# Kernel optimization log

Hardware: AMD Instinct MI355X
Metric: run time of the kernel (lower is better)

Reference implementation:

```python
import jax, jax.numpy as jnp
import numpy as np

N = 256
WINDOW = 16
HORIZON = 12
STEPS_PER_WEEK = 4
DT = 1.0 / STEPS_PER_WEEK


def setup_inputs() -> dict:
    key = jax.random.key(0)
    ks = jax.random.split(key, 8)
    B = 512
    x_hist = jax.random.uniform(ks[0], (B, WINDOW, N), dtype=jnp.float32)
    cnn_feat = jax.random.normal(ks[1], (B, 64), dtype=jnp.float32)
    s = 0.02  # small init scale to keep sigmoids/softmax well-behaved
    W1 = jax.random.normal(ks[2], (WINDOW * N, 128), dtype=jnp.float32) * s
    b1 = jnp.zeros((128,), jnp.float32)
    W2 = jax.random.normal(ks[3], (128, 4 * N), dtype=jnp.float32) * s
    b2 = jnp.zeros((4 * N,), jnp.float32)
    M1 = jax.random.normal(ks[4], (64, 128), dtype=jnp.float32) * s
    mb1 = jnp.zeros((128,), jnp.float32)
    M2 = jax.random.normal(ks[5], (128, N * N), dtype=jnp.float32) * s
    mb2 = jnp.zeros((N * N,), jnp.float32)
    return {"x_hist": x_hist, "cnn_feat": cnn_feat, "W1": W1, "b1": b1,
            "W2": W2, "b2": b2, "M1": M1, "mb1": mb1, "M2": M2, "mb2": mb2}


def reference(x_hist, cnn_feat, W1, b1, W2, b2, M1, mb1, M2, mb2):
    B, T, n = x_hist.shape
    # param_net: Linear -> ReLU -> Linear
    h = jax.nn.relu(x_hist.reshape(B, -1) @ W1 + b1)
    params = h @ W2 + b2  # (B, 4N)
    beta = jax.nn.sigmoid(params[:, :n]) * 3.0
    sigma = jax.nn.sigmoid(params[:, n:2 * n]) * 1.0
    gamma = jax.nn.sigmoid(params[:, 2 * n:3 * n]) * 1.0
    e0_ratio = jax.nn.sigmoid(params[:, 3 * n:]) * 5.0
    # mobility_net -> row-softmax mobility matrix Pi (B, N, N)
    hm = jax.nn.relu(cnn_feat @ M1 + mb1)
    Pi = jax.nn.softmax((hm @ M2 + mb2).reshape(B, n, n), axis=-1)

    I0 = jnp.maximum(x_hist[:, -1], 1e-6)
    E0 = I0 * e0_ratio
    S0 = jnp.maximum(1.0 - E0 - I0, 0.01)

    def get_grads(S, E, I):
        # bmm(I[:,None,:], Pi).squeeze(1) == einsum bn,bnm->bm
        force = jnp.einsum('bn,bnm->bm', I, Pi)
        new_inf = beta * S * force
        return -new_inf, new_inf - sigma * E, sigma * E - gamma * I

    def week_step(carry, _):
        S, E, I = carry
        for _ in range(STEPS_PER_WEEK):
            dS1, dE1, dI1 = get_grads(S, E, I)
            dS2, dE2, dI2 = get_grads(S + 0.5 * DT * dS1, E + 0.5 * DT * dE1, I + 0.5 * DT * dI1)
            dS3, dE3, dI3 = get_grads(S + 0.5 * DT * dS2, E + 0.5 * DT * dE2, I + 0.5 * DT * dI2)
            dS4, dE4, dI4 = get_grads(S + DT * dS3, E + DT * dE3, I + DT * dI3)
            S = jnp.clip(S + DT / 6.0 * (dS1 + 2 * dS2 + 2 * dS3 + dS4), 0.0, 1.0)
            E = jnp.clip(E + DT / 6.0 * (dE1 + 2 * dE2 + 2 * dE3 + dE4), 0.0, 1.0)
            I = jnp.clip(I + DT / 6.0 * (dI1 + 2 * dI2 + 2 * dI3 + dI4), 0.0, 1.0)
        return (S, E, I), (I, E)

    _, (I_s, E_s) = jax.lax.scan(week_step, (S0, E0, I0), None, length=HORIZON)
    I_sim = jnp.swapaxes(I_s, 0, 1)  # (B, horizon, N)
    E_sim = jnp.swapaxes(E_s, 0, 1)
    return (I_sim, E_sim, beta.mean(0), sigma.mean(0), gamma.mean(0), Pi.mean(0))
```

## Files before the change

### kernel.cpp

```cpp
#include <hip/hip_runtime.h>
#include <hip/hip_bf16.h>
#include <stdint.h>
#include <stddef.h>

typedef _Float16 half2_t __attribute__((ext_vector_type(2)));
typedef _Float16 f16x8 __attribute__((ext_vector_type(8)));
typedef float f32x4 __attribute__((ext_vector_type(4)));

__device__ __forceinline__ float fdot2(half2_t a, half2_t b, float c) {
#if __has_builtin(__builtin_amdgcn_fdot2)
  return __builtin_amdgcn_fdot2(a, b, c, false);
#else
  return c + (float)a.x * (float)b.x + (float)a.y * (float)b.y;
#endif
}

__global__ __launch_bounds__(128) void k_paramnet1(
    const float* __restrict__ X, const float* __restrict__ W1,
    float* __restrict__ hpart) {
  const int j = threadIdx.x;
  const int ks = blockIdx.x;
  const int b0 = blockIdx.y * 32;

  float w1r[128];
#pragma unroll
  for (int k = 0; k < 128; ++k)
    w1r[k] = W1[(size_t)(ks * 128 + k) * 128 + j];

  for (int bb = 0; bb < 32; ++bb) {
    const float* xr = X + (size_t)(b0 + bb) * 4096 + ks * 128;
    float a0 = 0.f, a1 = 0.f, a2 = 0.f, a3 = 0.f;
#pragma unroll
    for (int k = 0; k < 128; k += 4) {
      a0 = fmaf(w1r[k + 0], xr[k + 0], a0);
      a1 = fmaf(w1r[k + 1], xr[k + 1], a1);
      a2 = fmaf(w1r[k + 2], xr[k + 2], a2);
      a3 = fmaf(w1r[k + 3], xr[k + 3], a3);
    }
    hpart[((size_t)ks * 512 + (b0 + bb)) * 128 + j] = (a0 + a1) + (a2 + a3);
  }
}

__global__ __launch_bounds__(256) void k_paramnet2(
    const float* __restrict__ hpart, const float* __restrict__ b1,
    float* __restrict__ h) {
  const int idx = blockIdx.x * 256 + threadIdx.x;
  float s = b1[idx & 127];
#pragma unroll
  for (int ks = 0; ks < 32; ++ks) s += hpart[(size_t)ks * 65536 + idx];
  h[idx] = fmaxf(s, 0.f);
}

__global__ __launch_bounds__(256) void k_params_state(
    const float* __restrict__ h, const float* __restrict__ W2,
    const float* __restrict__ b2, const float* __restrict__ X,
    float* __restrict__ betaW, float* __restrict__ sigmaW,
    float* __restrict__ gammaW, float* __restrict__ S0W,
    float* __restrict__ E0W, float* __restrict__ I0W,
    float* __restrict__ stats) {
  const int b0 = blockIdx.x * 2;
  const int t = threadIdx.x;
  const float* h0 = h + (size_t)b0 * 128;
  const float* h1 = h0 + 128;
  float a00 = b2[t], a01 = b2[256 + t], a02 = b2[512 + t], a03 = b2[768 + t];
  float a10 = a00, a11 = a01, a12 = a02, a13 = a03;
#pragma unroll 2
  for (int k = 0; k < 128; ++k) {
    const float* wr = W2 + (size_t)k * 1024;
    const float w0 = wr[t], w1 = wr[256 + t], w2 = wr[512 + t], w3 = wr[768 + t];
    const float hv0 = h0[k], hv1 = h1[k];
    a00 = fmaf(hv0, w0, a00); a01 = fmaf(hv0, w1, a01);
    a02 = fmaf(hv0, w2, a02); a03 = fmaf(hv0, w3, a03);
    a10 = fmaf(hv1, w0, a10); a11 = fmaf(hv1, w1, a11);
    a12 = fmaf(hv1, w2, a12); a13 = fmaf(hv1, w3, a13);
  }
  float bsum = 0.f, ssum = 0.f, gsum = 0.f;
#pragma unroll
  for (int j = 0; j < 2; ++j) {
    const float p0 = j ? a10 : a00, p1 = j ? a11 : a01;
    const float p2 = j ? a12 : a02, p3 = j ? a13 : a03;
    const float beta = 3.f / (1.f + __expf(-p0));
    const float sig  = 1.f / (1.f + __expf(-p1));
    const float gam  = 1.f / (1.f + __expf(-p2));
    const float e0r  = 5.f / (1.f + __expf(-p3));
    const int base = (b0 + j) * 256 + t;
    const float I0 = fmaxf(X[(size_t)(b0 + j) * 4096 + 15 * 256 + t], 1e-6f);
    const float E0 = I0 * e0r;
    const float S0 = fmaxf(1.f - E0 - I0, 0.01f);
    betaW[base] = beta; sigmaW[base] = sig; gammaW[base] = gam;
    S0W[base] = S0; E0W[base] = E0; I0W[base] = I0;
    bsum += beta; ssum += sig; gsum += gam;
  }
  atomicAdd(stats + t, bsum);
  atomicAdd(stats + 256 + t, ssum);
  atomicAdd(stats + 512 + t, gsum);
}

__global__ __launch_bounds__(128) void k_mobility1(
    const float* __restrict__ cnn, const float* __restrict__ M1,
    const float* __restrict__ mb1, _Float16* __restrict__ hmf) {
  const int b = blockIdx.x, j = threadIdx.x;
  const float* cr = cnn + b * 64;
  float a = mb1[j];
#pragma unroll
  for (int k = 0; k < 64; ++k) a = fmaf(cr[k], M1[k * 128 + j], a);
  hmf[b * 128 + j] = (_Float16)fmaxf(a, 0.f);
}

__global__ __launch_bounds__(256) void k_cvtM2(
    const float* __restrict__ M2, _Float16* __restrict__ M2T) {
  const int n = blockIdx.x, t = threadIdx.x;
  __shared__ _Float16 sm[128 * 256];
  const float* src = M2 + (size_t)n * 256 + t;
#pragma unroll 8
  for (int k = 0; k < 128; ++k)
    sm[k * 256 + t] = (_Float16)src[(size_t)k * 65536];
  __syncthreads();
  half2_t col[64];
#pragma unroll 16
  for (int k2 = 0; k2 < 64; ++k2)
    col[k2] = half2_t{sm[(2 * k2) * 256 + t], sm[(2 * k2 + 1) * 256 + t]};
  uint4* dst = (uint4*)(M2T + ((size_t)n * 256 + t) * 128);
  const uint4* s4 = (const uint4*)col;
#pragma unroll
  for (int i = 0; i < 16; ++i) dst[i] = s4[i];
}

__global__ __launch_bounds__(512, 2) void k_mobility2(
    const _Float16* __restrict__ hmf, const _Float16* __restrict__ M2T,
    const float* __restrict__ mb2, _Float16* __restrict__ PiF,
    float* __restrict__ pimpart) {
  const int n = blockIdx.x;
  const int pass = blockIdx.y;
  const int tid = threadIdx.x;
  const int wave = tid >> 6;
  const int lane = tid & 63;
  const int q = lane >> 4;
  const int c = lane & 15;

  __shared__ _Float16 sm[8][16 * 256];

  const _Float16* Bbase = M2T + (size_t)n * 32768 + (size_t)c * 128 + q * 8;
  const float* mbp = mb2 + n * 256 + c;

  const int bt0 = wave * 4 + pass * 2;
  f32x4 C0[16], C1[16];
#pragma unroll
  for (int nb = 0; nb < 16; ++nb) {
    const float mbv = mbp[nb * 16];
    C0[nb] = f32x4{mbv, mbv, mbv, mbv};
    C1[nb] = C0[nb];
  }
  const _Float16* A0 = hmf + (size_t)(bt0 * 16 + c) * 128 + q * 8;
  const _Float16* A1 = A0 + 16 * 128;
#pragma unroll
  for (int ks = 0; ks < 4; ++ks) {
    const f16x8 Af0 = *(const f16x8*)(A0 + ks * 32);
    const f16x8 Af1 = *(const f16x8*)(A1 + ks * 32);
#pragma unroll
    for (int nb = 0; nb < 16; ++nb) {
      const f16x8 Bf = *(const f16x8*)(Bbase + nb * 2048 + ks * 32);
      C0[nb] = __builtin_amdgcn_mfma_f32_16x16x32_f16(Af0, Bf, C0[nb], 0, 0, 0);
      C1[nb] = __builtin_amdgcn_mfma_f32_16x16x32_f16(Af1, Bf, C1[nb], 0, 0, 0);
    }
  }

  float colsum[16];
#pragma unroll
  for (int nb = 0; nb < 16; ++nb) colsum[nb] = 0.f;

#pragma unroll
  for (int half = 0; half < 2; ++half) {
    f32x4* C = half ? C1 : C0;
    const int bt = bt0 + half;
    float mx[4], sum[4];
#pragma unroll
    for (int r = 0; r < 4; ++r) mx[r] = C[0][r];
#pragma unroll
    for (int nb = 1; nb < 16; ++nb)
#pragma unroll
      for (int r = 0; r < 4; ++r) mx[r] = fmaxf(mx[r], C[nb][r]);
#pragma unroll
    for (int r = 0; r < 4; ++r) {
      mx[r] = fmaxf(mx[r], __shfl_xor(mx[r], 1, 16));
      mx[r] = fmaxf(mx[r], __shfl_xor(mx[r], 2, 16));
      mx[r] = fmaxf(mx[r], __shfl_xor(mx[r], 4, 16));
      mx[r] = fmaxf(mx[r], __shfl_xor(mx[r], 8, 16));
      sum[r] = 0.f;
    }
#pragma unroll
    for (int nb = 0; nb < 16; ++nb)
#pragma unroll
      for (int r = 0; r < 4; ++r) {
        const float e = __expf(C[nb][r] - mx[r]);
        C[nb][r] = e;
        sum[r] += e;
      }
#pragma unroll
    for (int r = 0; r < 4; ++r) {
      sum[r] += __shfl_xor(sum[r], 1, 16);
      sum[r] += __shfl_xor(sum[r], 2, 16);
      sum[r] += __shfl_xor(sum[r], 4, 16);
      sum[r] += __shfl_xor(sum[r], 8, 16);
      sum[r] = 1.f / sum[r];
    }
    _Float16* slot = sm[wave];
#pragma unroll
    for (int nb = 0; nb < 16; ++nb) {
#pragma unroll
      for (int r = 0; r < 4; ++r) {
        const float v = C[nb][r] * sum[r];
        colsum[nb] += v;
        slot[(q * 4 + r) * 256 + nb * 16 + c] = (_Float16)v;
      }
    }
    const int l2 = lane & 31, rh = lane >> 5;
    _Float16* Pg = PiF + ((size_t)(bt * 16) * 256 + n) * 256;
#pragma unroll
    for (int i = 0; i < 8; ++i) {
      const int row = i * 2 + rh;
      const uint4 v = *(const uint4*)(slot + row * 256 + l2 * 8);
      *(uint4*)(Pg + (size_t)row * 65536 + l2 * 8) = v;
    }
  }
#pragma unroll
  for (int nb = 0; nb < 16; ++nb) {
    colsum[nb] += __shfl_xor(colsum[nb], 16);
    colsum[nb] += __shfl_xor(colsum[nb], 32);
  }
  if (lane < 16) {
    float* pp = pimpart + n * 256 + lane;
#pragma unroll
    for (int nb = 0; nb < 16; ++nb) atomicAdd(pp + nb * 16, colsum[nb]);
  }
}

__global__ __launch_bounds__(256) void k_finalize(
    const float* __restrict__ stats, const float* __restrict__ pimpart,
    float* __restrict__ out) {
  const int idx = blockIdx.x * 256 + threadIdx.x;
  const float inv = 1.f / 512.f;
  if (idx < 768) {
    out[3145728 + idx] = stats[idx] * inv;
  } else {
    const int pm = idx - 768;
    out[3146496 + pm] = pimpart[pm] * inv;
  }
}

__global__ __launch_bounds__(512, 4) void k_sim(
    const _Float16* __restrict__ PiF, const float* __restrict__ betaW,
    const float* __restrict__ sigmaW, const float* __restrict__ gammaW,
    const float* __restrict__ S0W, const float* __restrict__ E0W,
    const float* __restrict__ I0W, float* __restrict__ out) {
  const int b = blockIdx.x;
  const int tid = threadIdx.x;
  const int w = tid >> 6, lane = tid & 63;
  const int q = lane >> 4, c = lane & 15;
  const int iown = q >> 1;
  const int mown = (2 * w + iown) * 16 + c;

  __shared__ __align__(16) _Float16 Ib[2][256];

  f16x8 Bf[2][8];
  {
    const _Float16* P = PiF + (size_t)b * 65536 + (size_t)(q * 8) * 256 + c;
#pragma unroll
    for (int i = 0; i < 2; ++i) {
#pragma unroll
      for (int t = 0; t < 8; ++t) {
        const _Float16* src = P + (size_t)(t * 32) * 256 + (2 * w + i) * 16;
        f16x8 v;
#pragma unroll
        for (int j = 0; j < 8; ++j) v[j] = src[(size_t)j * 256];
        Bf[i][t] = v;
      }
    }
  }

  const int base = b * 256 + mown;
  const float bet = betaW[base], sig = sigmaW[base], gam = gammaW[base];
  float S = S0W[base], E = E0W[base], I = I0W[base];

  int p = 0;
  auto grads = [&](float Ss, float Es, float Is, float& dS, float& dE, float& dI) {
    Ib[p][mown] = (_Float16)Is;
    __syncthreads();
    const f16x8* ia = (const f16x8*)Ib[p];
    p ^= 1;
    f32x4 C0 = f32x4{0.f, 0.f, 0.f, 0.f};
    f32x4 C1 = f32x4{0.f, 0.f, 0.f, 0.f};
#pragma unroll
    for (int t = 0; t < 8; ++t) {
      const f16x8 A = ia[t * 4 + q];
      C0 = __builtin_amdgcn_mfma_f32_16x16x32_f16(A, Bf[0][t], C0, 0, 0, 0);
      C1 = __builtin_amdgcn_mfma_f32_16x16x32_f16(A, Bf[1][t], C1, 0, 0, 0);
    }
    const float force = iown ? C1[0] : C0[0];
    const float ninf = bet * Ss * force;
    const float sE = sig * Es;
    dS = -ninf;
    dE = ninf - sE;
    dI = sE - gam * Is;
  };

  float* outI = out + (size_t)b * (12 * 256) + mown;
  float* outE = outI + 1572864;
  const float c6 = 0.25f / 6.f;

  for (int wk = 0; wk < 12; ++wk) {
    for (int st = 0; st < 4; ++st) {
      float d1S, d1E, d1I, d2S, d2E, d2I, d3S, d3E, d3I, d4S, d4E, d4I;
      grads(S, E, I, d1S, d1E, d1I);
      grads(S + 0.125f * d1S, E + 0.125f * d1E, I + 0.125f * d1I, d2S, d2E, d2I);
      grads(S + 0.125f * d2S, E + 0.125f * d2E, I + 0.125f * d2I, d3S, d3E, d3I);
      grads(S + 0.25f * d3S, E + 0.25f * d3E, I + 0.25f * d3I, d4S, d4E, d4I);
      S = fminf(fmaxf(S + c6 * (d1S + 2.f * d2S + 2.f * d3S + d4S), 0.f), 1.f);
      E = fminf(fmaxf(E + c6 * (d1E + 2.f * d2E + 2.f * d3E + d4E), 0.f), 1.f);
      I = fminf(fmaxf(I + c6 * (d1I + 2.f * d2I + 2.f * d3I + d4I), 0.f), 1.f);
    }
    if ((q & 1) == 0) {
      outI[wk * 256] = I;
      outE[wk * 256] = E;
    }
  }
}

extern "C" void kernel_launch(void* const* d_in, const int* in_sizes, int n_in,
                              void* d_out, int out_size, void* d_ws, size_t ws_size,
                              hipStream_t stream) {
  const float* x_hist = (const float*)d_in[0];
  const float* cnn    = (const float*)d_in[1];
  const float* W1     = (const float*)d_in[2];
  const float* b1     = (const float*)d_in[3];
  const float* W2     = (const float*)d_in[4];
  const float* b2     = (const float*)d_in[5];
  const float* M1     = (const float*)d_in[6];
  const float* mb1    = (const float*)d_in[7];
  const float* M2     = (const float*)d_in[8];
  const float* mb2    = (const float*)d_in[9];
  float* out = (float*)d_out;

  char* w = (char*)d_ws;
  _Float16* M2T     = (_Float16*)(w + 0);
  _Float16* hmf     = (_Float16*)(w + 16777216);
  float*    betaW   = (float*)(w + 16908288);
  float*    sigmaW  = (float*)(w + 17432576);
  float*    gammaW  = (float*)(w + 17956864);
  float*    S0W     = (float*)(w + 18481152);
  float*    E0W     = (float*)(w + 19005440);
  float*    I0W     = (float*)(w + 19529728);
  float*    pimpart = (float*)(w + 20054016);
  float*    stats   = (float*)(w + 20316160);
  _Float16* PiF     = (_Float16*)(w + 20320256);
  float*    hpart   = (float*)(w + 20320256);
  float*    h       = (float*)(w + 28708864);

  hipMemsetAsync(pimpart, 0, 266240, stream);
  k_paramnet1<<<dim3(32, 16), 128, 0, stream>>>(x_hist, W1, hpart);
  k_paramnet2<<<256, 256, 0, stream>>>(hpart, b1, h);
  k_params_state<<<256, 256, 0, stream>>>(h, W2, b2, x_hist, betaW, sigmaW,
                                          gammaW, S0W, E0W, I0W, stats);
  k_mobility1<<<512, 128, 0, stream>>>(cnn, M1, mb1, hmf);
  k_cvtM2<<<256, 256, 0, stream>>>(M2, M2T);
  k_mobility2<<<dim3(256, 2), 512, 0, stream>>>(hmf, M2T, mb2, PiF, pimpart);
  k_finalize<<<259, 256, 0, stream>>>(stats, pimpart, out);
  k_sim<<<512, 512, 0, stream>>>(PiF, betaW, sigmaW, gammaW, S0W, E0W, I0W, out);
}
```

Measured before the change: 458.3 us.

## Process two batch elements per block in SEIR simulation kernel

Each block of the RK4 simulation kernel now handles two batch samples. Both mobility matrices are held in registers, and interleaved MFMA chains share a single barrier per gradient evaluation. This is meant to amortise the synchronisation and latency cost of the serial time-stepping loop across two independent problems. In exchange it doubles register use, lowers the occupancy bound, and halves the grid size.

Result: no change. 464.4 us (+1.3%).

```diff
diff --git a/kernel.cpp b/kernel.cpp
--- a/kernel.cpp
+++ b/kernel.cpp
@@ -248,80 +248,113 @@
   }
 }
 
-__global__ __launch_bounds__(512, 4) void k_sim(
+__global__ __launch_bounds__(512, 2) void k_sim(
     const _Float16* __restrict__ PiF, const float* __restrict__ betaW,
     const float* __restrict__ sigmaW, const float* __restrict__ gammaW,
     const float* __restrict__ S0W, const float* __restrict__ E0W,
     const float* __restrict__ I0W, float* __restrict__ out) {
-  const int b = blockIdx.x;
+  const int b0 = blockIdx.x * 2;
   const int tid = threadIdx.x;
   const int w = tid >> 6, lane = tid & 63;
   const int q = lane >> 4, c = lane & 15;
   const int iown = q >> 1;
   const int mown = (2 * w + iown) * 16 + c;
 
-  __shared__ __align__(16) _Float16 Ib[2][256];
-
-  f16x8 Bf[2][8];
+  __shared__ __align__(16) _Float16 IbL[2][2][256];
+
+  f16x8 Bf[2][2][8];
   {
-    const _Float16* P = PiF + (size_t)b * 65536 + (size_t)(q * 8) * 256 + c;
-#pragma unroll
-    for (int i = 0; i < 2; ++i) {
-#pragma unroll
-      for (int t = 0; t < 8; ++t) {
-        const _Float16* src = P + (size_t)(t * 32) * 256 + (2 * w + i) * 16;
-        f16x8 v;
-#pragma unroll
-        for (int j = 0; j < 8; ++j) v[j] = src[(size_t)j * 256];
-        Bf[i][t] = v;
+#pragma unroll
+    for (int bj = 0; bj < 2; ++bj) {
+      const _Float16* P =
+          PiF + (size_t)(b0 + bj) * 65536 + (size_t)(q * 8) * 256 + c;
+#pragma unroll
+      for (int i = 0; i < 2; ++i) {
+#pragma unroll
+        for (int t = 0; t < 8; ++t) {
+          const _Float16* src = P + (size_t)(t * 32) * 256 + (2 * w + i) * 16;
+          f16x8 v;
+#pragma unroll
+          for (int j = 0; j < 8; ++j) v[j] = src[(size_t)j * 256];
+          Bf[bj][i][t] = v;
+        }
       }
     }
   }
 
-  const int base = b * 256 + mown;
-  const float bet = betaW[base], sig = sigmaW[base], gam = gammaW[base];
-  float S = S0W[base], E = E0W[base], I = I0W[base];
+  const int baseA = (b0 + 0) * 256 + mown;
+  const int baseB = (b0 + 1) * 256 + mown;
+  const float betA = betaW[baseA], sigA = sigmaW[baseA], gamA = gammaW[baseA];
+  const float betB = betaW[baseB], sigB = sigmaW[baseB], gamB = gammaW[baseB];
+  float SA = S0W[baseA], EA = E0W[baseA], IA = I0W[baseA];
+  float SB = S0W[baseB], EB = E0W[baseB], IB = I0W[baseB];
 
   int p = 0;
-  auto grads = [&](float Ss, float Es, float Is, float& dS, float& dE, float& dI) {
-    Ib[p][mown] = (_Float16)Is;
+  auto grads = [&](float Sa, float Ea, float Ia, float Sb, float Eb, float Iv,
+                   float& dSa, float& dEa, float& dIa,
+                   float& dSb, float& dEb, float& dIb) {
+    IbL[p][0][mown] = (_Float16)Ia;
+    IbL[p][1][mown] = (_Float16)Iv;
     __syncthreads();
-    const f16x8* ia = (const f16x8*)Ib[p];
+    const f16x8* ia0 = (const f16x8*)IbL[p][0];
+    const f16x8* ia1 = (const f16x8*)IbL[p][1];
     p ^= 1;
-    f32x4 C0 = f32x4{0.f, 0.f, 0.f, 0.f};
-    f32x4 C1 = f32x4{0.f, 0.f, 0.f, 0.f};
+    f32x4 C00 = f32x4{0.f, 0.f, 0.f, 0.f};
+    f32x4 C01 = C00, C10 = C00, C11 = C00;
 #pragma unroll
     for (int t = 0; t < 8; ++t) {
-      const f16x8 A = ia[t * 4 + q];
-      C0 = __builtin_amdgcn_mfma_f32_16x16x32_f16(A, Bf[0][t], C0, 0, 0, 0);
-      C1 = __builtin_amdgcn_mfma_f32_16x16x32_f16(A, Bf[1][t], C1, 0, 0, 0);
-    }
-    const float force = iown ? C1[0] : C0[0];
-    const float ninf = bet * Ss * force;
-    const float sE = sig * Es;
-    dS = -ninf;
-    dE = ninf - sE;
-    dI = sE - gam * Is;
+      const f16x8 A0 = ia0[t * 4 + q];
+      const f16x8 A1 = ia1[t * 4 + q];
+      C00 = __builtin_amdgcn_mfma_f32_16x16x32_f16(A0, Bf[0][0][t], C00, 0, 0, 0);
+      C01 = __builtin_amdgcn_mfma_f32_16x16x32_f16(A0, Bf[0][1][t], C01, 0, 0, 0);
+      C10 = __builtin_amdgcn_mfma_f32_16x16x32_f16(A1, Bf[1][0][t], C10, 0, 0, 0);
+      C11 = __builtin_amdgcn_mfma_f32_16x16x32_f16(A1, Bf[1][1][t], C11, 0, 0, 0);
+    }
+    const float fa = iown ? C01[0] : C00[0];
+    const float fb = iown ? C11[0] : C10[0];
+    const float ninfa = betA * Sa * fa;
+    const float sEa = sigA * Ea;
+    dSa = -ninfa; dEa = ninfa - sEa; dIa = sEa - gamA * Ia;
+    const float ninfb = betB * Sb * fb;
+    const float sEb = sigB * Eb;
+    dSb = -ninfb; dEb = ninfb - sEb; dIb = sEb - gamB * Iv;
   };
 
-  float* outI = out + (size_t)b * (12 * 256) + mown;
-  float* outE = outI + 1572864;
+  float* outIA = out + (size_t)(b0 + 0) * 3072 + mown;
+  float* outEA = outIA + 1572864;
+  float* outIB = out + (size_t)(b0 + 1) * 3072 + mown;
+  float* outEB = outIB + 1572864;
   const float c6 = 0.25f / 6.f;
 
   for (int wk = 0; wk < 12; ++wk) {
     for (int st = 0; st < 4; ++st) {
-      float d1S, d1E, d1I, d2S, d2E, d2I, d3S, d3E, d3I, d4S, d4E, d4I;
-      grads(S, E, I, d1S, d1E, d1I);
-      grads(S + 0.125f * d1S, E + 0.125f * d1E, I + 0.125f * d1I, d2S, d2E, d2I);
-      grads(S + 0.125f * d2S, E + 0.125f * d2E, I + 0.125f * d2I, d3S, d3E, d3I);
-      grads(S + 0.25f * d3S, E + 0.25f * d3E, I + 0.25f * d3I, d4S, d4E, d4I);
-      S = fminf(fmaxf(S + c6 * (d1S + 2.f * d2S + 2.f * d3S + d4S), 0.f), 1.f);
-      E = fminf(fmaxf(E + c6 * (d1E + 2.f * d2E + 2.f * d3E + d4E), 0.f), 1.f);
-      I = fminf(fmaxf(I + c6 * (d1I + 2.f * d2I + 2.f * d3I + d4I), 0.f), 1.f);
+      float d1Sa, d1Ea, d1Ia, d1Sb, d1Eb, d1Ib;
+      float d2Sa, d2Ea, d2Ia, d2Sb, d2Eb, d2Ib;
+      float d3Sa, d3Ea, d3Ia, d3Sb, d3Eb, d3Ib;
+      float d4Sa, d4Ea, d4Ia, d4Sb, d4Eb, d4Ib;
+      grads(SA, EA, IA, SB, EB, IB,
+            d1Sa, d1Ea, d1Ia, d1Sb, d1Eb, d1Ib);
+      grads(SA + 0.125f * d1Sa, EA + 0.125f * d1Ea, IA + 0.125f * d1Ia,
+            SB + 0.125f * d1Sb, EB + 0.125f * d1Eb, IB + 0.125f * d1Ib,
+            d2Sa, d2Ea, d2Ia, d2Sb, d2Eb, d2Ib);
+      grads(SA + 0.125f * d2Sa, EA + 0.125f * d2Ea, IA + 0.125f * d2Ia,
+            SB + 0.125f * d2Sb, EB + 0.125f * d2Eb, IB + 0.125f * d2Ib,
+            d3Sa, d3Ea, d3Ia, d3Sb, d3Eb, d3Ib);
+      grads(SA + 0.25f * d3Sa, EA + 0.25f * d3Ea, IA + 0.25f * d3Ia,
+            SB + 0.25f * d3Sb, EB + 0.25f * d3Eb, IB + 0.25f * d3Ib,
+            d4Sa, d4Ea, d4Ia, d4Sb, d4Eb, d4Ib);
+      SA = fminf(fmaxf(SA + c6 * (d1Sa + 2.f * d2Sa + 2.f * d3Sa + d4Sa), 0.f), 1.f);
+      EA = fminf(fmaxf(EA + c6 * (d1Ea + 2.f * d2Ea + 2.f * d3Ea + d4Ea), 0.f), 1.f);
+      IA = fminf(fmaxf(IA + c6 * (d1Ia + 2.f * d2Ia + 2.f * d3Ia + d4Ia), 0.f), 1.f);
+      SB = fminf(fmaxf(SB + c6 * (d1Sb + 2.f * d2Sb + 2.f * d3Sb + d4Sb), 0.f), 1.f);
+      EB = fminf(fmaxf(EB + c6 * (d1Eb + 2.f * d2Eb + 2.f * d3Eb + d4Eb), 0.f), 1.f);
+      IB = fminf(fmaxf(IB + c6 * (d1Ib + 2.f * d2Ib + 2.f * d3Ib + d4Ib), 0.f), 1.f);
     }
     if ((q & 1) == 0) {
-      outI[wk * 256] = I;
-      outE[wk * 256] = E;
+      outIA[wk * 256] = IA;
+      outEA[wk * 256] = EA;
+      outIB[wk * 256] = IB;
+      outEB[wk * 256] = EB;
     }
   }
 }
@@ -365,5 +398,5 @@
   k_cvtM2<<<256, 256, 0, stream>>>(M2, M2T);
   k_mobility2<<<dim3(256, 2), 512, 0, stream>>>(hmf, M2T, mb2, PiF, pimpart);
   k_finalize<<<259, 256, 0, stream>>>(stats, pimpart, out);
-  k_sim<<<512, 512, 0, stream>>>(PiF, betaW, sigmaW, gammaW, S0W, E0W, I0W, out);
-}
+  k_sim<<<256, 512, 0, stream>>>(PiF, betaW, sigmaW, gammaW, S0W, E0W, I0W, out);
+}
```
